# Performance work log

Measured on AMD Instinct MI355X. Metric: run time of the kernel, lower is better.

## Reference

```python
import jax, jax.numpy as jnp
import numpy as np

B, Q_LEN, HIDDEN, N_HEADS, HEAD_DIM = 8, 256, 4096, 32, 128
BLOCK_SIZE, BLOCKS_PER_SEQ, NUM_BLOCKS = 64, 12, 96
MAX_HIST = 512
ROPE_BASE = 10000.0


def setup_inputs() -> dict:
    key = jax.random.key(0)
    ks = jax.random.split(key, 8)
    hidden_states = jax.random.normal(ks[0], (1, B * Q_LEN, HIDDEN), jnp.float32)
    c_attn_w = jax.random.normal(ks[1], (3 * HIDDEN, HIDDEN), jnp.float32) * 0.02
    c_attn_b = jax.random.normal(ks[2], (3 * HIDDEN,), jnp.float32) * 0.02
    c_proj_w = jax.random.normal(ks[3], (HIDDEN, HIDDEN), jnp.float32) * 0.02
    k_cache = jax.random.normal(ks[4], (NUM_BLOCKS, BLOCK_SIZE, N_HEADS, HEAD_DIM), jnp.float32)
    v_cache = jax.random.normal(ks[5], (NUM_BLOCKS, BLOCK_SIZE, N_HEADS, HEAD_DIM), jnp.float32)
    history_lengths = jax.random.randint(ks[6], (B,), 0, MAX_HIST)
    block_offsets = jnp.arange(B * BLOCKS_PER_SEQ, dtype=jnp.int32).reshape(B, BLOCKS_PER_SEQ)
    return dict(hidden_states=hidden_states, c_attn_w=c_attn_w, c_attn_b=c_attn_b,
                c_proj_w=c_proj_w, k_cache=k_cache, v_cache=v_cache,
                history_lengths=history_lengths, block_offsets=block_offsets)


def _rotate_half(x):
    x1, x2 = x[..., :HEAD_DIM // 2], x[..., HEAD_DIM // 2:]
    return jnp.concatenate([-x2, x1], axis=-1)


def reference(hidden_states, c_attn_w, c_attn_b, c_proj_w, k_cache, v_cache,
              history_lengths, block_offsets):
    T = B * Q_LEN  # total tokens (continuous batching, flattened)
    x = hidden_states[0]  # [T, HIDDEN]
    # fused QKV projection
    qkv = x @ c_attn_w.T + c_attn_b  # [T, 3*HIDDEN]
    q, k, v = jnp.split(qkv, 3, axis=-1)
    q = q.reshape(T, N_HEADS, HEAD_DIM)
    k = k.reshape(T, N_HEADS, HEAD_DIM)
    v = v.reshape(T, N_HEADS, HEAD_DIM)
    # per-token absolute positions (position_ids_1d)
    positions = (history_lengths[:, None] + jnp.arange(Q_LEN)).reshape(-1)  # [T]
    # RoPE (ntk_alpha = 1)
    inv_freq = 1.0 / (ROPE_BASE ** (jnp.arange(0, HEAD_DIM, 2, dtype=jnp.float32) / HEAD_DIM))
    freqs = positions.astype(jnp.float32)[:, None] * inv_freq  # [T, D/2]
    emb = jnp.concatenate([freqs, freqs], axis=-1)  # [T, D]
    cos, sin = jnp.cos(emb)[:, None, :], jnp.sin(emb)[:, None, :]

    def rope(t):
        tf = t.astype(jnp.float32)
        return (tf * cos + _rotate_half(tf) * sin).astype(t.dtype)

    q, k = rope(q), rope(k)
    # fill_kv_cache: scatter new K/V into paged blocks at slot = position
    seq_ids = jnp.repeat(jnp.arange(B), Q_LEN)  # [T]
    blk = block_offsets[seq_ids, positions // BLOCK_SIZE]  # [T]
    slot = positions % BLOCK_SIZE  # [T]
    k_cache = k_cache.at[blk, slot].set(k)
    v_cache = v_cache.at[blk, slot].set(v)
    # paged attention: gather each sequence's blocks -> [B, KV, H, D]
    KV = BLOCKS_PER_SEQ * BLOCK_SIZE
    keys = k_cache[block_offsets].reshape(B, KV, N_HEADS, HEAD_DIM)
    vals = v_cache[block_offsets].reshape(B, KV, N_HEADS, HEAD_DIM)
    q_b = q.reshape(B, Q_LEN, N_HEADS, HEAD_DIM)
    scale = 1.0 / jnp.sqrt(jnp.asarray(HEAD_DIM, jnp.float32))
    scores = jnp.einsum('bqhd,bkhd->bhqk', q_b, keys) * scale  # [B,H,Q,KV]
    q_global = history_lengths[:, None] + jnp.arange(Q_LEN)  # [B,Q]
    causal = jnp.arange(KV)[None, None, :] <= q_global[:, :, None]  # [B,Q,KV]
    scores = jnp.where(causal[:, None, :, :], scores, jnp.finfo(scores.dtype).min)
    probs = jax.nn.softmax(scores, axis=-1)
    attn = jnp.einsum('bhqk,bkhd->bqhd', probs, vals).reshape(T, HIDDEN)
    out = attn @ c_proj_w.T  # c_proj (bias-free)
    return out.reshape(1, T, HIDDEN)
```

## Files before the change

### kernel.cpp

```cpp
#include <hip/hip_runtime.h>

typedef unsigned short ushort_t;
typedef float f32x4 __attribute__((ext_vector_type(4)));
typedef _Float16 f16x8 __attribute__((ext_vector_type(8)));
typedef short s16x8 __attribute__((ext_vector_type(8)));

#define NB 8
#define QL 256
#define HID 4096
#define NH 32
#define HD 128

__device__ __forceinline__ _Float16 f2h(float f) { return (_Float16)f; }
__device__ __forceinline__ ushort_t h2u(_Float16 h) {
  union { _Float16 h; ushort_t u; } x; x.h = h; return x.u;
}
__device__ __forceinline__ float u2f(ushort_t u) {
  union { _Float16 h; ushort_t u; } x; x.u = u; return (float)x.h;
}

#define MFMA16H(a, b, c) __builtin_amdgcn_mfma_f32_16x16x32_f16((a), (b), (c), 0, 0, 0)
#define AS1 __attribute__((address_space(1)))
#define AS3 __attribute__((address_space(3)))
#define VMCNT(n) asm volatile("s_waitcnt vmcnt(" #n ")" ::: "memory")
#define NOSTG

__global__ __launch_bounds__(256)
void conv_tile(const float* __restrict__ src, ushort_t* __restrict__ dst,
               int K, int ntiles) {
  const int tile = blockIdx.x * 4 + (threadIdx.x >> 6);
  if (tile >= ntiles) return;
  const int u = threadIdx.x & 63;
  const int row = u >> 2, seg = u & 3;
  const int K32 = K >> 5;
  const int mb = tile / K32, kb = tile % K32;
  const float* sp = src + (size_t)(mb * 16 + row) * K + kb * 32 + seg * 8;
  ushort_t t[8];
#pragma unroll
  for (int j = 0; j < 8; ++j) t[j] = h2u(f2h(sp[j]));
  *(s16x8*)(dst + (size_t)tile * 512 + (((seg << 4) | row) * 8)) = *(s16x8*)t;
}

template<int NT>
__global__ __launch_bounds__(256, 2)
void gemm_qkv(const ushort_t* __restrict__ At, const ushort_t* __restrict__ Bt,
              const float* __restrict__ bias, ushort_t* __restrict__ Ch,
              int N) {
  static_assert(NT % 3 == 2 && NT >= 8, "tail assumes NT%3==2");
  extern __shared__ ushort_t lds[];
  const int nwg = gridDim.x, bid = blockIdx.x;
  const int wg = (bid & 7) * (nwg >> 3) + (bid >> 3);
  const int mi = wg & 7, ni = wg >> 3;
  const int tid = threadIdx.x, w = tid >> 6, l = tid & 63;
  const int l16 = l & 15, lg = l >> 4;
  const int wm = w >> 1, wn = w & 1;

  const ushort_t* sA[4];
  const ushort_t* sB[2];
#pragma unroll
  for (int i = 0; i < 4; ++i)
    sA[i] = At + ((size_t)(mi * 16 + 4 * w + i) * NT) * 512 + l * 8;
#pragma unroll
  for (int i = 0; i < 2; ++i)
    sB[i] = Bt + ((size_t)(ni * 8 + 2 * w + i) * NT) * 512 + l * 8;

  int aof[8], bof[4];
#pragma unroll
  for (int mf = 0; mf < 8; ++mf) aof[mf] = (wm * 8 + mf) * 512 + l * 8;
#pragma unroll
  for (int nf = 0; nf < 4; ++nf) bof[nf] = 8192 + (wn * 4 + nf) * 512 + l * 8;

  f32x4 acc[8][4];
#pragma unroll
  for (int m = 0; m < 8; ++m)
#pragma unroll
    for (int n = 0; n < 4; ++n) acc[m][n] = (f32x4){0.f, 0.f, 0.f, 0.f};

#define GLDS(srcp, dstofs)                                                    \
  __builtin_amdgcn_global_load_lds((const AS1 void*)(srcp),                   \
                                   (AS3 void*)&lds[dstofs], 16, 0, 0)
#define STGQ(R, J)                                                            \
  do {                                                                        \
    GLDS(sA[0] + (size_t)(J) * 512, (R) * 12288 + (4 * w + 0) * 512);         \
    GLDS(sA[1] + (size_t)(J) * 512, (R) * 12288 + (4 * w + 1) * 512);         \
    GLDS(sA[2] + (size_t)(J) * 512, (R) * 12288 + (4 * w + 2) * 512);         \
    GLDS(sA[3] + (size_t)(J) * 512, (R) * 12288 + (4 * w + 3) * 512);         \
    GLDS(sB[0] + (size_t)(J) * 512, (R) * 12288 + 8192 + (2 * w + 0) * 512);  \
    GLDS(sB[1] + (size_t)(J) * 512, (R) * 12288 + 8192 + (2 * w + 1) * 512);  \
  } while (0)

#define ITERQ(R, VMW, STGCODE)                                                \
  do {                                                                        \
    VMW;                                                                      \
    __builtin_amdgcn_s_barrier();                                             \
    STGCODE;                                                                  \
    f16x8 fa[8], fb[4];                                                       \
    _Pragma("unroll") for (int mf = 0; mf < 8; ++mf)                          \
        fa[mf] = *(const f16x8*)&lds[(R) * 12288 + aof[mf]];                  \
    _Pragma("unroll") for (int nf = 0; nf < 4; ++nf)                          \
        fb[nf] = *(const f16x8*)&lds[(R) * 12288 + bof[nf]];                  \
    asm volatile("s_waitcnt lgkmcnt(0)" ::: "memory");                        \
    __builtin_amdgcn_sched_barrier(0);                                        \
    __builtin_amdgcn_s_setprio(1);                                            \
    _Pragma("unroll") for (int mf = 0; mf < 8; ++mf)                          \
    _Pragma("unroll") for (int nf = 0; nf < 4; ++nf)                          \
        acc[mf][nf] = MFMA16H(fa[mf], fb[nf], acc[mf][nf]);                   \
    __builtin_amdgcn_s_setprio(0);                                            \
  } while (0)

  STGQ(0, 0);
  STGQ(1, 1);
  for (int j = 0; j < NT - 2; j += 3) {
    ITERQ(0, VMCNT(6), STGQ(2, j + 2));
    ITERQ(1, VMCNT(6), STGQ(0, j + 3));
    ITERQ(2, VMCNT(6), STGQ(1, j + 4));
  }
  ITERQ(0, VMCNT(6), NOSTG);
  ITERQ(1, VMCNT(0), NOSTG);

#pragma unroll
  for (int nf = 0; nf < 4; ++nf) {
    const int col = ni * 128 + wn * 64 + nf * 16 + l16;
    const float bi = bias[col];
#pragma unroll
    for (int mf = 0; mf < 8; ++mf) {
      const int row0 = mi * 256 + wm * 128 + mf * 16 + lg * 4;
#pragma unroll
      for (int rr = 0; rr < 4; ++rr)
        Ch[(size_t)(row0 + rr) * N + col] = h2u(f2h(acc[mf][nf][rr] + bi));
    }
  }
#undef STGQ
#undef ITERQ
}

template<int NT>
__global__ __launch_bounds__(256, 3)
void gemm_proj(const ushort_t* __restrict__ At, const ushort_t* __restrict__ Bt,
               float* __restrict__ Cf, int N) {
  static_assert(NT % 3 == 2 && NT >= 8, "tail assumes NT%3==2");
  extern __shared__ ushort_t lds[];
  const int nwg = gridDim.x, bid = blockIdx.x;
  const int wg = (bid & 7) * (nwg >> 3) + (bid >> 3);
  const int mi = wg & 15, ni = wg >> 4;
  const int tid = threadIdx.x, w = tid >> 6, l = tid & 63;
  const int l16 = l & 15, lg = l >> 4;
  const int wm = w >> 1, wn = w & 1;

  const ushort_t* sA0 = At + ((size_t)(mi * 8 + 2 * w) * NT) * 512 + l * 8;
  const ushort_t* sA1 = At + ((size_t)(mi * 8 + 2 * w + 1) * NT) * 512 + l * 8;
  const ushort_t* sB0 = Bt + ((size_t)(ni * 8 + 2 * w) * NT) * 512 + l * 8;
  const ushort_t* sB1 = Bt + ((size_t)(ni * 8 + 2 * w + 1) * NT) * 512 + l * 8;

  int aof[4], bof[4];
#pragma unroll
  for (int mf = 0; mf < 4; ++mf) aof[mf] = (wm * 4 + mf) * 512 + l * 8;
#pragma unroll
  for (int nf = 0; nf < 4; ++nf) bof[nf] = 4096 + (wn * 4 + nf) * 512 + l * 8;

  f32x4 acc[4][4];
#pragma unroll
  for (int m = 0; m < 4; ++m)
#pragma unroll
    for (int n = 0; n < 4; ++n) acc[m][n] = (f32x4){0.f, 0.f, 0.f, 0.f};

#define STGP(R, J)                                                            \
  do {                                                                        \
    GLDS(sA0 + (size_t)(J) * 512, (R) * 8192 + (2 * w) * 512);                \
    GLDS(sA1 + (size_t)(J) * 512, (R) * 8192 + (2 * w + 1) * 512);            \
    GLDS(sB0 + (size_t)(J) * 512, (R) * 8192 + 4096 + (2 * w) * 512);         \
    GLDS(sB1 + (size_t)(J) * 512, (R) * 8192 + 4096 + (2 * w + 1) * 512);     \
  } while (0)

#define ITERP(R, VMW, STGCODE)                                                \
  do {                                                                        \
    VMW;                                                                      \
    __builtin_amdgcn_s_barrier();                                             \
    STGCODE;                                                                  \
    f16x8 fa[4], fb[4];                                                       \
    _Pragma("unroll") for (int mf = 0; mf < 4; ++mf)                          \
        fa[mf] = *(const f16x8*)&lds[(R) * 8192 + aof[mf]];                   \
    _Pragma("unroll") for (int nf = 0; nf < 4; ++nf)                          \
        fb[nf] = *(const f16x8*)&lds[(R) * 8192 + bof[nf]];                   \
    asm volatile("s_waitcnt lgkmcnt(0)" ::: "memory");                        \
    __builtin_amdgcn_sched_barrier(0);                                        \
    __builtin_amdgcn_s_setprio(1);                                            \
    _Pragma("unroll") for (int mf = 0; mf < 4; ++mf)                          \
    _Pragma("unroll") for (int nf = 0; nf < 4; ++nf)                          \
        acc[mf][nf] = MFMA16H(fa[mf], fb[nf], acc[mf][nf]);                   \
    __builtin_amdgcn_s_setprio(0);                                            \
  } while (0)

  STGP(0, 0);
  STGP(1, 1);
  for (int j = 0; j < NT - 2; j += 3) {
    ITERP(0, VMCNT(4), STGP(2, j + 2));
    ITERP(1, VMCNT(4), STGP(0, j + 3));
    ITERP(2, VMCNT(4), STGP(1, j + 4));
  }
  ITERP(0, VMCNT(4), NOSTG);
  ITERP(1, VMCNT(0), NOSTG);

#pragma unroll
  for (int nf = 0; nf < 4; ++nf) {
    const int col = ni * 128 + wn * 64 + nf * 16 + l16;
#pragma unroll
    for (int mf = 0; mf < 4; ++mf) {
      const int row0 = mi * 128 + wm * 64 + mf * 16 + lg * 4;
#pragma unroll
      for (int rr = 0; rr < 4; ++rr)
        Cf[(size_t)(row0 + rr) * N + col] = acc[mf][nf][rr];
    }
  }
#undef STGP
#undef ITERP
}

__global__ __launch_bounds__(256)
void rope_inplace(ushort_t* __restrict__ qkv, const int* __restrict__ hist) {
  const int t = blockIdx.x;
  const int b = t >> 8, qq = t & 255;
  __shared__ float cs[64], sn[64];
  const int tid = threadIdx.x;
  if (tid < 64) {
    const float pos = (float)(hist[b] + qq);
    const float f = pos * __expf(-(float)tid * (9.210340371976184f / 64.0f));
    cs[tid] = cosf(f);
    sn[tid] = sinf(f);
  }
  __syncthreads();
  ushort_t* row = qkv + (size_t)t * 12288;
  const int h = tid >> 3;
  const int j0 = (tid & 7) * 8;
  const float qscale = 0.08838834764831845f;
  float c[8], s[8];
#pragma unroll
  for (int j = 0; j < 8; ++j) { c[j] = cs[j0 + j]; s[j] = sn[j0 + j]; }
  {
    ushort_t* p1 = row + h * HD + j0;
    ushort_t* p2 = p1 + 64;
    s16x8 a = *(s16x8*)p1, bb = *(s16x8*)p2;
    ushort_t o1[8], o2[8];
#pragma unroll
    for (int j = 0; j < 8; ++j) {
      const float x1 = u2f((ushort_t)a[j]), x2 = u2f((ushort_t)bb[j]);
      o1[j] = h2u(f2h((x1 * c[j] - x2 * s[j]) * qscale));
      o2[j] = h2u(f2h((x2 * c[j] + x1 * s[j]) * qscale));
    }
    *(s16x8*)p1 = *(s16x8*)o1;
    *(s16x8*)p2 = *(s16x8*)o2;
  }
  {
    ushort_t* p1 = row + HID + h * HD + j0;
    ushort_t* p2 = p1 + 64;
    s16x8 a = *(s16x8*)p1, bb = *(s16x8*)p2;
    ushort_t o1[8], o2[8];
#pragma unroll
    for (int j = 0; j < 8; ++j) {
      const float x1 = u2f((ushort_t)a[j]), x2 = u2f((ushort_t)bb[j]);
      o1[j] = h2u(f2h(x1 * c[j] - x2 * s[j]));
      o2[j] = h2u(f2h(x2 * c[j] + x1 * s[j]));
    }
    *(s16x8*)p1 = *(s16x8*)o1;
    *(s16x8*)p2 = *(s16x8*)o2;
  }
}

__global__ __launch_bounds__(512, 2)
void attn_fwd(const ushort_t* __restrict__ qkv,
              const float* __restrict__ k_cache, const float* __restrict__ v_cache,
              const int* __restrict__ hist, const int* __restrict__ bofs,
              ushort_t* __restrict__ attn_t) {
  const int bh = blockIdx.x;
  const int b = bh >> 5, h = bh & 31;
  const int hb = hist[b];

  __shared__ ushort_t K_lds[64 * 136];
  __shared__ ushort_t V_lds[128 * 72];
  __shared__ ushort_t P_lds[256 * 72];

  const int tid = threadIdx.x;
  const int w = tid >> 6, l = tid & 63;
  const int l16 = l & 15, lg = l >> 4;

  f16x8 qf[2][4];
#pragma unroll
  for (int m = 0; m < 2; ++m) {
    const int qrow = w * 32 + m * 16 + l16;
    const ushort_t* qp = qkv + (size_t)(b * QL + qrow) * 12288 + h * HD + lg * 8;
#pragma unroll
    for (int kd = 0; kd < 4; ++kd) qf[m][kd] = *(const f16x8*)(qp + kd * 32);
  }

  f32x4 o[2][8];
  float mr[2][4], sr[2][4];
#pragma unroll
  for (int m = 0; m < 2; ++m) {
#pragma unroll
    for (int d = 0; d < 8; ++d) o[m][d] = (f32x4){0.f, 0.f, 0.f, 0.f};
#pragma unroll
    for (int r = 0; r < 4; ++r) { mr[m][r] = -1e30f; sr[m][r] = 0.f; }
  }

  const int nt = (hb + QL + 63) >> 6;
  const int srow = tid >> 4;
  const int seg = tid & 15;

  for (int t = 0; t < nt; ++t) {
    const int kv0 = t << 6;
    __syncthreads();
#pragma unroll
    for (int p = 0; p < 2; ++p) {
      const int row = p * 32 + srow;
      const int kvg = kv0 + row;
      if (kvg < hb) {
        const int blk = bofs[b * 12 + t];
        const size_t base = ((size_t)blk * 64 + (kvg & 63)) * HID + h * HD;
        const float* kf = k_cache + base;
        const float* vf = v_cache + base;
        ushort_t tmp[8];
#pragma unroll
        for (int j = 0; j < 8; ++j) tmp[j] = h2u(f2h(kf[seg * 8 + j]));
        *(s16x8*)&K_lds[row * 136 + seg * 8] = *(s16x8*)tmp;
#pragma unroll
        for (int j = 0; j < 8; ++j) {
          const int d = seg + j * 16;
          V_lds[d * 72 + row] = h2u(f2h(vf[d]));
        }
      } else {
        int r2 = kvg - hb;
        if (r2 > QL - 1) r2 = QL - 1;
        const size_t base = (size_t)(b * QL + r2) * 12288 + h * HD;
        const ushort_t* kb = qkv + base + HID;
        const ushort_t* vb = qkv + base + 2 * HID;
        *(s16x8*)&K_lds[row * 136 + seg * 8] = *(const s16x8*)(kb + seg * 8);
#pragma unroll
        for (int j = 0; j < 8; ++j) {
          const int d = seg + j * 16;
          V_lds[d * 72 + row] = vb[d];
        }
      }
    }
    __syncthreads();

    f32x4 sa[2][4];
#pragma unroll
    for (int m = 0; m < 2; ++m)
#pragma unroll
      for (int n = 0; n < 4; ++n) sa[m][n] = (f32x4){0.f, 0.f, 0.f, 0.f};
#pragma unroll
    for (int kd = 0; kd < 4; ++kd) {
      f16x8 kf[4];
#pragma unroll
      for (int n = 0; n < 4; ++n)
        kf[n] = *(const f16x8*)&K_lds[(n * 16 + l16) * 136 + kd * 32 + lg * 8];
#pragma unroll
      for (int m = 0; m < 2; ++m)
#pragma unroll
        for (int n = 0; n < 4; ++n)
          sa[m][n] = MFMA16H(qf[m][kd], kf[n], sa[m][n]);
    }

#pragma unroll
    for (int m = 0; m < 2; ++m) {
#pragma unroll
      for (int n = 0; n < 4; ++n) {
        const int kvg = kv0 + n * 16 + l16;
#pragma unroll
        for (int r = 0; r < 4; ++r) {
          const int qg = hb + w * 32 + m * 16 + lg * 4 + r;
          if (kvg > qg) sa[m][n][r] = -1e30f;
        }
      }
      float tm[4], ts[4];
#pragma unroll
      for (int r = 0; r < 4; ++r)
        tm[r] = fmaxf(fmaxf(sa[m][0][r], sa[m][1][r]),
                      fmaxf(sa[m][2][r], sa[m][3][r]));
#pragma unroll
      for (int x = 1; x < 16; x <<= 1)
#pragma unroll
        for (int r = 0; r < 4; ++r)
          tm[r] = fmaxf(tm[r], __shfl_xor(tm[r], x, 16));
#pragma unroll
      for (int r = 0; r < 4; ++r) {
        const float nm = fmaxf(mr[m][r], tm[r]);
        const float corr = __expf(mr[m][r] - nm);
        mr[m][r] = nm;
        sr[m][r] *= corr;
#pragma unroll
        for (int d = 0; d < 8; ++d) o[m][d][r] *= corr;
        ts[r] = 0.f;
      }
#pragma unroll
      for (int n = 0; n < 4; ++n)
#pragma unroll
        for (int r = 0; r < 4; ++r) {
          const float p = __expf(sa[m][n][r] - mr[m][r]);
          sa[m][n][r] = p;
          ts[r] += p;
        }
#pragma unroll
      for (int x = 1; x < 16; x <<= 1)
#pragma unroll
        for (int r = 0; r < 4; ++r) ts[r] += __shfl_xor(ts[r], x, 16);
#pragma unroll
      for (int r = 0; r < 4; ++r) sr[m][r] += ts[r];
#pragma unroll
      for (int n = 0; n < 4; ++n)
#pragma unroll
        for (int r = 0; r < 4; ++r)
          P_lds[(w * 32 + m * 16 + lg * 4 + r) * 72 + n * 16 + l16] =
              h2u(f2h(sa[m][n][r]));
    }

#pragma unroll
    for (int ks = 0; ks < 2; ++ks) {
      f16x8 pa[2];
#pragma unroll
      for (int m = 0; m < 2; ++m)
        pa[m] = *(const f16x8*)&P_lds[(w * 32 + m * 16 + l16) * 72 + ks * 32 + lg * 8];
#pragma unroll
      for (int d = 0; d < 8; ++d) {
        const f16x8 vb =
            *(const f16x8*)&V_lds[(d * 16 + l16) * 72 + ks * 32 + lg * 8];
#pragma unroll
        for (int m = 0; m < 2; ++m) o[m][d] = MFMA16H(pa[m], vb, o[m][d]);
      }
    }
  }

#pragma unroll
  for (int m = 0; m < 2; ++m) {
    const int rb = b * 16 + w * 2 + m;
#pragma unroll
    for (int r = 0; r < 4; ++r) {
      const float inv = 1.0f / sr[m][r];
#pragma unroll
      for (int d = 0; d < 8; ++d) {
        const int kb = h * 4 + (d >> 1);
        const int lane_dst = (lg * 4 + r) | ((((d & 1) << 1) | (l16 >> 3)) << 4);
        attn_t[((size_t)(rb * 128 + kb)) * 512 + lane_dst * 8 + (l16 & 7)] =
            h2u(f2h(o[m][d][r] * inv));
      }
    }
  }
}

extern "C" void kernel_launch(void* const* d_in, const int* in_sizes, int n_in,
                              void* d_out, int out_size, void* d_ws,
                              size_t ws_size, hipStream_t stream) {
  const float* hidden   = (const float*)d_in[0];
  const float* c_attn_w = (const float*)d_in[1];
  const float* c_attn_b = (const float*)d_in[2];
  const float* c_proj_w = (const float*)d_in[3];
  const float* k_cache  = (const float*)d_in[4];
  const float* v_cache  = (const float*)d_in[5];
  const int* hist       = (const int*)d_in[6];
  const int* bofs       = (const int*)d_in[7];
  float* out = (float*)d_out;

  char* ws = (char*)d_ws;
  const size_t MB = 1ull << 20;
  ushort_t* w_attn_t = (ushort_t*)(ws);
  ushort_t* wproj_t  = (ushort_t*)(ws);
  ushort_t* qkv_h   = (ushort_t*)(ws + 100 * MB);
  ushort_t* attn_t  = (ushort_t*)(ws + 148 * MB);
  ushort_t* x_t     = (ushort_t*)(ws + 196 * MB);

  conv_tile<<<4096, 256, 0, stream>>>(hidden, x_t, 4096, 16384);
  conv_tile<<<24576, 256, 0, stream>>>(c_attn_w, w_attn_t, 4096, 98304);
  gemm_qkv<128><<<768, 256, 73728, stream>>>(x_t, w_attn_t, c_attn_b, qkv_h,
                                             12288);
  rope_inplace<<<2048, 256, 0, stream>>>(qkv_h, hist);
  conv_tile<<<8192, 256, 0, stream>>>(c_proj_w, wproj_t, 4096, 32768);
  attn_fwd<<<256, 512, 0, stream>>>(qkv_h, k_cache, v_cache, hist, bofs,
                                    attn_t);
  gemm_proj<128><<<512, 256, 49152, stream>>>(attn_t, wproj_t, out, 4096);
}
```

Baseline: 414.2 us.

## Load QKV GEMM A-fragments directly into registers, stage only B through LDS

The QKV GEMM now loads each wave's A fragments straight from global memory into double-buffered registers one k-tile ahead, and only the B tile goes through LDS via global_load_lds. LDS use drops from 72KB to 24KB per workgroup and the A LDS reads go away. In exchange, waves sharing the same wm each fetch the same A data redundantly from global/L2, register pressure rises with two 8-fragment A buffers, and the main loop is unrolled by six to alternate the buffers.

```diff
diff --git a/kernel.cpp b/kernel.cpp
--- a/kernel.cpp
+++ b/kernel.cpp
@@ -46,7 +46,7 @@
 void gemm_qkv(const ushort_t* __restrict__ At, const ushort_t* __restrict__ Bt,
               const float* __restrict__ bias, ushort_t* __restrict__ Ch,
               int N) {
-  static_assert(NT % 3 == 2 && NT >= 8, "tail assumes NT%3==2");
+  static_assert(NT % 6 == 2 && NT >= 14, "main loop covers NT-2 tiles, %6==0");
   extern __shared__ ushort_t lds[];
   const int nwg = gridDim.x, bid = blockIdx.x;
   const int wg = (bid & 7) * (nwg >> 3) + (bid >> 3);
@@ -55,68 +55,68 @@
   const int l16 = l & 15, lg = l >> 4;
   const int wm = w >> 1, wn = w & 1;
 
-  const ushort_t* sA[4];
-  const ushort_t* sB[2];
-#pragma unroll
-  for (int i = 0; i < 4; ++i)
-    sA[i] = At + ((size_t)(mi * 16 + 4 * w + i) * NT) * 512 + l * 8;
-#pragma unroll
-  for (int i = 0; i < 2; ++i)
-    sB[i] = Bt + ((size_t)(ni * 8 + 2 * w + i) * NT) * 512 + l * 8;
-
-  int aof[8], bof[4];
-#pragma unroll
-  for (int mf = 0; mf < 8; ++mf) aof[mf] = (wm * 8 + mf) * 512 + l * 8;
-#pragma unroll
-  for (int nf = 0; nf < 4; ++nf) bof[nf] = 8192 + (wn * 4 + nf) * 512 + l * 8;
+  const ushort_t* sA[8];
+#pragma unroll
+  for (int mf = 0; mf < 8; ++mf)
+    sA[mf] = At + ((size_t)(mi * 16 + wm * 8 + mf) * NT) * 512 + l * 8;
+  const ushort_t* sB0 = Bt + ((size_t)(ni * 8 + 2 * w) * NT) * 512 + l * 8;
+  const ushort_t* sB1 = Bt + ((size_t)(ni * 8 + 2 * w + 1) * NT) * 512 + l * 8;
+
+  int bof[4];
+#pragma unroll
+  for (int nf = 0; nf < 4; ++nf) bof[nf] = (wn * 4 + nf) * 512 + l * 8;
 
   f32x4 acc[8][4];
 #pragma unroll
   for (int m = 0; m < 8; ++m)
 #pragma unroll
     for (int n = 0; n < 4; ++n) acc[m][n] = (f32x4){0.f, 0.f, 0.f, 0.f};
+
+  f16x8 a0[8], a1[8];
 
 #define GLDS(srcp, dstofs)                                                    \
   __builtin_amdgcn_global_load_lds((const AS1 void*)(srcp),                   \
                                    (AS3 void*)&lds[dstofs], 16, 0, 0)
-#define STGQ(R, J)                                                            \
+#define STGB(R, J)                                                            \
   do {                                                                        \
-    GLDS(sA[0] + (size_t)(J) * 512, (R) * 12288 + (4 * w + 0) * 512);         \
-    GLDS(sA[1] + (size_t)(J) * 512, (R) * 12288 + (4 * w + 1) * 512);         \
-    GLDS(sA[2] + (size_t)(J) * 512, (R) * 12288 + (4 * w + 2) * 512);         \
-    GLDS(sA[3] + (size_t)(J) * 512, (R) * 12288 + (4 * w + 3) * 512);         \
-    GLDS(sB[0] + (size_t)(J) * 512, (R) * 12288 + 8192 + (2 * w + 0) * 512);  \
-    GLDS(sB[1] + (size_t)(J) * 512, (R) * 12288 + 8192 + (2 * w + 1) * 512);  \
+    GLDS(sB0 + (size_t)(J) * 512, (R) * 4096 + (2 * w) * 512);                \
+    GLDS(sB1 + (size_t)(J) * 512, (R) * 4096 + (2 * w + 1) * 512);            \
   } while (0)
-
-#define ITERQ(R, VMW, STGCODE)                                                \
+#define LDA(DST, J)                                                           \
+  _Pragma("unroll") for (int mf = 0; mf < 8; ++mf)                            \
+      DST[mf] = *(const f16x8*)(sA[mf] + (size_t)(J) * 512)
+#define POSQ(R, ACUR, VMW, LDACODE, STGCODE)                                  \
   do {                                                                        \
     VMW;                                                                      \
     __builtin_amdgcn_s_barrier();                                             \
+    LDACODE;                                                                  \
     STGCODE;                                                                  \
-    f16x8 fa[8], fb[4];                                                       \
-    _Pragma("unroll") for (int mf = 0; mf < 8; ++mf)                          \
-        fa[mf] = *(const f16x8*)&lds[(R) * 12288 + aof[mf]];                  \
+    f16x8 fb[4];                                                              \
     _Pragma("unroll") for (int nf = 0; nf < 4; ++nf)                          \
-        fb[nf] = *(const f16x8*)&lds[(R) * 12288 + bof[nf]];                  \
+        fb[nf] = *(const f16x8*)&lds[(R) * 4096 + bof[nf]];                   \
     asm volatile("s_waitcnt lgkmcnt(0)" ::: "memory");                        \
     __builtin_amdgcn_sched_barrier(0);                                        \
     __builtin_amdgcn_s_setprio(1);                                            \
     _Pragma("unroll") for (int mf = 0; mf < 8; ++mf)                          \
     _Pragma("unroll") for (int nf = 0; nf < 4; ++nf)                          \
-        acc[mf][nf] = MFMA16H(fa[mf], fb[nf], acc[mf][nf]);                   \
+        acc[mf][nf] = MFMA16H(ACUR[mf], fb[nf], acc[mf][nf]);                 \
     __builtin_amdgcn_s_setprio(0);                                            \
   } while (0)
 
-  STGQ(0, 0);
-  STGQ(1, 1);
-  for (int j = 0; j < NT - 2; j += 3) {
-    ITERQ(0, VMCNT(6), STGQ(2, j + 2));
-    ITERQ(1, VMCNT(6), STGQ(0, j + 3));
-    ITERQ(2, VMCNT(6), STGQ(1, j + 4));
-  }
-  ITERQ(0, VMCNT(6), NOSTG);
-  ITERQ(1, VMCNT(0), NOSTG);
+  LDA(a0, 0);
+  STGB(0, 0);
+  STGB(1, 1);
+
+  for (int j = 0; j < NT - 2; j += 6) {
+    POSQ(0, a0, VMCNT(2), LDA(a1, j + 1), STGB(2, j + 2));
+    POSQ(1, a1, VMCNT(2), LDA(a0, j + 2), STGB(0, j + 3));
+    POSQ(2, a0, VMCNT(2), LDA(a1, j + 3), STGB(1, j + 4));
+    POSQ(0, a1, VMCNT(2), LDA(a0, j + 4), STGB(2, j + 5));
+    POSQ(1, a0, VMCNT(2), LDA(a1, j + 5), STGB(0, j + 6));
+    POSQ(2, a1, VMCNT(2), LDA(a0, j + 6), STGB(1, j + 7));
+  }
+  POSQ(0, a0, VMCNT(2), LDA(a1, NT - 1), NOSTG);
+  POSQ(1, a1, VMCNT(0), NOSTG, NOSTG);
 
 #pragma unroll
   for (int nf = 0; nf < 4; ++nf) {
@@ -130,8 +130,9 @@
         Ch[(size_t)(row0 + rr) * N + col] = h2u(f2h(acc[mf][nf][rr] + bi));
     }
   }
-#undef STGQ
-#undef ITERQ
+#undef STGB
+#undef LDA
+#undef POSQ
 }
 
 template<int NT>
@@ -470,7 +471,7 @@
 
   conv_tile<<<4096, 256, 0, stream>>>(hidden, x_t, 4096, 16384);
   conv_tile<<<24576, 256, 0, stream>>>(c_attn_w, w_attn_t, 4096, 98304);
-  gemm_qkv<128><<<768, 256, 73728, stream>>>(x_t, w_attn_t, c_attn_b, qkv_h,
+  gemm_qkv<128><<<768, 256, 24576, stream>>>(x_t, w_attn_t, c_attn_b, qkv_h,
                                              12288);
   rope_inplace<<<2048, 256, 0, stream>>>(qkv_h, hist);
   conv_tile<<<8192, 256, 0, stream>>>(c_proj_w, wproj_t, 4096, 32768);
```

Result: slower. 499.4 us (+20.6%).
